# Performance work log

Measured on AMD Instinct MI355X. Metric: run time of the kernel, lower is better.

## Reference

```python
import jax, jax.numpy as jnp
import numpy as np

# ---------- static mesh topology helpers (numpy, setup-time only) ----------

def _topo_subdivide(nv, faces):
    edge_id = {}
    mids = []
    nf = []
    def mid(a, b):
        k = (a, b) if a < b else (b, a)
        if k not in edge_id:
            edge_id[k] = nv + len(mids)
            mids.append(k)
        return edge_id[k]
    for a, b, c in faces:
        a, b, c = int(a), int(b), int(c)
        ab, bc, ca = mid(a, b), mid(b, c), mid(c, a)
        nf += [[a, ab, ca], [b, bc, ab], [c, ca, bc], [ab, bc, ca]]
    return np.array(nf, dtype=np.int64), np.array(mids, dtype=np.int64)

def _icosphere(level, radius):
    t = (1.0 + 5.0 ** 0.5) / 2.0
    v = np.array([[-1, t, 0], [1, t, 0], [-1, -t, 0], [1, -t, 0],
                  [0, -1, t], [0, 1, t], [0, -1, -t], [0, 1, -t],
                  [t, 0, -1], [t, 0, 1], [-t, 0, -1], [-t, 0, 1]], dtype=np.float64)
    v /= np.linalg.norm(v, axis=1, keepdims=True)
    f = np.array([[0, 11, 5], [0, 5, 1], [0, 1, 7], [0, 7, 10], [0, 10, 11],
                  [1, 5, 9], [5, 11, 4], [11, 10, 2], [10, 7, 6], [7, 1, 8],
                  [3, 9, 4], [3, 4, 2], [3, 2, 6], [3, 6, 8], [3, 8, 9],
                  [4, 9, 5], [2, 4, 11], [6, 2, 10], [8, 6, 7], [9, 8, 1]], dtype=np.int64)
    for _ in range(level):
        f, mids = _topo_subdivide(len(v), f)
        mv = v[mids[:, 0]] + v[mids[:, 1]]
        mv /= np.linalg.norm(mv, axis=1, keepdims=True)
        v = np.concatenate([v, mv], 0)
    return (v * radius).astype(np.float32), f

def _directed_edges(faces):
    e = np.concatenate([faces[:, [0, 1]], faces[:, [1, 2]], faces[:, [2, 0]],
                        faces[:, [1, 0]], faces[:, [2, 1]], faces[:, [0, 2]]], 0)
    return np.unique(e, axis=0).T.astype(np.int64)  # (2, E) directed, deduped

# ---------- jax forward math ----------

def _project(verts, camera_c, camera_f):
    # K @ [I | t], t = (0,0,0.8): rows [f0,0,c0,0.8*c0],[0,f1,c1,0.8*c1],[0,0,1,0.8]
    z = jnp.zeros((), verts.dtype); o = jnp.ones((), verts.dtype)
    tz = jnp.asarray(0.8, verts.dtype)
    P = jnp.stack([
        jnp.stack([camera_f[0], z, camera_c[0], tz * camera_c[0]]),
        jnp.stack([z, camera_f[1], camera_c[1], tz * camera_c[1]]),
        jnp.stack([z, z, o, tz])])
    hom = jnp.concatenate([verts, jnp.ones((verts.shape[0], 1), verts.dtype)], 1)
    pc = hom @ P.T                     # (V, 3)
    return pc[:, :2] / pc[:, 2:3]      # (V, 2) pixel coords [x, y]

def _bilerp(feat, px, py, image_size):
    # feat: (C, dim, dim); px, py: (V,)
    dim = feat.shape[1]
    x = px * dim / image_size
    y = py * dim / image_size
    x1 = jnp.floor(x); x2 = x1 + 1.0
    y1 = jnp.floor(y); y2 = y1 + 1.0
    xi1 = jnp.clip(x1.astype(jnp.int32), 0, dim - 1)
    xi2 = jnp.clip(x2.astype(jnp.int32), 0, dim - 1)
    yi1 = jnp.clip(y1.astype(jnp.int32), 0, dim - 1)
    yi2 = jnp.clip(y2.astype(jnp.int32), 0, dim - 1)
    f11 = feat[:, xi1, yi1].T  # (V, C)
    f12 = feat[:, xi1, yi2].T
    f21 = feat[:, xi2, yi1].T
    f22 = feat[:, xi2, yi2].T
    w11 = ((x2 - x) * (y2 - y))[:, None]
    w12 = ((x2 - x) * (y - y1))[:, None]
    w21 = ((x - x1) * (y2 - y))[:, None]
    w22 = ((x - x1) * (y - y1))[:, None]
    return w11 * f11 + w12 * f12 + w21 * f21 + w22 * f22

def _gconv(x, W0, W1, b, src, dst):
    agg = jax.ops.segment_sum(x[dst], src, num_segments=x.shape[0])
    return x @ W0 + agg @ W1 + b

def _gresnet(x, edges, params):
    Win0, Win1, bin_, W0s, W1s, bs, Wc0, Wc1, bc = params
    src, dst = edges[0], edges[1]
    h = jax.nn.relu(_gconv(x, Win0, Win1, bin_, src, dst))
    def body(h, lw):
        W0, W1, b = lw
        return jax.nn.relu(_gconv(h, W0, W1, b, src, dst)) + h, None
    h, _ = jax.lax.scan(body, h, (W0s, W1s, bs))
    coords = _gconv(h, Wc0, Wc1, bc, src, dst)
    return h, coords

def _forward(f3, f4, f5, verts0, camera_c, camera_f, p1, p2, p3,
             edges1, edges2, edges3, mid0, mid1, image_size):
    def deform(verts, shape_feat, edges, params):
        pix = _project(verts, camera_c, camera_f)
        px, py = pix[:, 0], pix[:, 1]
        perc = jnp.concatenate([_bilerp(f3, px, py, image_size),
                                _bilerp(f4, px, py, image_size),
                                _bilerp(f5, px, py, image_size)], 1)  # (V, 1280)
        feats = jnp.concatenate([perc, shape_feat], 1)
        h, coords = _gresnet(feats, edges, params)
        return coords, h
    def unpool(verts, feat, mid):
        vf = jnp.concatenate([verts, feat], 1)
        new = (vf[mid[:, 0]] + vf[mid[:, 1]]) * 0.5  # edge midpoints
        vf = jnp.concatenate([vf, new], 0)
        return vf[:, :3], vf[:, 3:]
    verts, feat = deform(verts0, verts0, edges1, p1)
    verts, feat = unpool(verts, feat, mid0)
    verts, feat = deform(verts, feat, edges2, p2)
    verts, feat = unpool(verts, feat, mid1)
    verts, _ = deform(verts, feat, edges3, p3)
    return verts  # (40962, 3)

# ---------- harness entry points ----------

def setup_inputs() -> dict:
    key = jax.random.key(0)
    keys = iter(jax.random.split(key, 64))
    v0, f0 = _icosphere(4, 0.2)                      # 2562 verts, 5120 faces
    f1, mid0 = _topo_subdivide(len(v0), f0)          # -> 10242 verts topology
    f2, mid1 = _topo_subdivide(len(v0) + len(mid0), f1)  # -> 40962 verts
    inp = {
        'f3': jax.random.normal(next(keys), (256, 56, 56), jnp.float32),
        'f4': jax.random.normal(next(keys), (512, 28, 28), jnp.float32),
        'f5': jax.random.normal(next(keys), (512, 14, 14), jnp.float32),
        'verts0': jnp.asarray(v0),
        'camera_c': jnp.array([112.0, 112.0], jnp.float32),
        'camera_f': jnp.array([248.0, 248.0], jnp.float32),
    }
    D, L = 128, 12
    def stage(prefix, in_dim):
        def w(shape, scale):
            return jax.random.normal(next(keys), shape, jnp.float32) * scale
        inp[prefix + '_Win0'] = w((in_dim, D), 1.0 / np.sqrt(in_dim))
        inp[prefix + '_Win1'] = w((in_dim, D), 1.0 / np.sqrt(in_dim))
        inp[prefix + '_bin'] = jnp.zeros((D,), jnp.float32)
        inp[prefix + '_W0'] = w((L, D, D), 0.3 / np.sqrt(D))
        inp[prefix + '_W1'] = w((L, D, D), 0.3 / np.sqrt(D))
        inp[prefix + '_b'] = jnp.zeros((L, D), jnp.float32)
        inp[prefix + '_Wc0'] = w((D, 3), 0.01 / np.sqrt(D))
        inp[prefix + '_Wc1'] = w((D, 3), 0.01 / np.sqrt(D))
        inp[prefix + '_bc'] = jnp.zeros((3,), jnp.float32)
    stage('g1', 1283)
    stage('g2', 1408)
    stage('g3', 1408)
    inp['edges1'] = jnp.asarray(_directed_edges(f0))   # (2, 15360)
    inp['edges2'] = jnp.asarray(_directed_edges(f1))   # (2, 61440)
    inp['edges3'] = jnp.asarray(_directed_edges(f2))   # (2, 245760)
    inp['mid0'] = jnp.asarray(mid0)                    # (7680, 2)
    inp['mid1'] = jnp.asarray(mid1)                    # (30720, 2)
    inp['image_size'] = 224
    return inp

def reference(f3, f4, f5, verts0, camera_c, camera_f,
              g1_Win0, g1_Win1, g1_bin, g1_W0, g1_W1, g1_b, g1_Wc0, g1_Wc1, g1_bc,
              g2_Win0, g2_Win1, g2_bin, g2_W0, g2_W1, g2_b, g2_Wc0, g2_Wc1, g2_bc,
              g3_Win0, g3_Win1, g3_bin, g3_W0, g3_W1, g3_b, g3_Wc0, g3_Wc1, g3_bc,
              edges1, edges2, edges3, mid0, mid1, image_size):
    p1 = (g1_Win0, g1_Win1, g1_bin, g1_W0, g1_W1, g1_b, g1_Wc0, g1_Wc1, g1_bc)
    p2 = (g2_Win0, g2_Win1, g2_bin, g2_W0, g2_W1, g2_b, g2_Wc0, g2_Wc1, g2_bc)
    p3 = (g3_Win0, g3_Win1, g3_bin, g3_W0, g3_W1, g3_b, g3_Wc0, g3_Wc1, g3_bc)
    return _forward(f3, f4, f5, verts0, camera_c, camera_f, p1, p2, p3,
                    edges1, edges2, edges3, mid0, mid1, image_size)
```

## Files before the change

kernel.cpp:

```cpp
#include <hip/hip_runtime.h>
#include <hip/hip_bf16.h>
#include <cstddef>
#include <cstdint>

#define DIV_UP(a, b) (((a) + (b) - 1) / (b))

typedef __attribute__((ext_vector_type(8))) short bf16x8v;
typedef __attribute__((ext_vector_type(4))) float f32x4v;

__device__ __forceinline__ unsigned short bf16_rn(float v) {
    unsigned int u = __float_as_uint(v);
    unsigned int r = (u + 0x7FFFu + ((u >> 16) & 1u)) >> 16;
    return (unsigned short)r;
}
__device__ __forceinline__ float bf16_f(unsigned short h) {
    return __uint_as_float(((unsigned int)h) << 16);
}
__device__ __forceinline__ void f2hl(float v, unsigned short& hi, unsigned short& lo) {
    hi = bf16_rn(v);
    float r = v - bf16_f(hi);
    lo = bf16_rn(r);
}
__device__ __forceinline__ int xcd_swz(int orig, int nwg) {
    int q = nwg >> 3, r = nwg & 7;
    int xcd = orig & 7, idx = orig >> 3;
    return (xcd < r ? xcd * (q + 1) : r * (q + 1) + (xcd - r) * q) + idx;
}

__global__ void transpose_hl(const float* __restrict__ in, unsigned short* __restrict__ ohi,
                             unsigned short* __restrict__ olo, int C, int HW) {
    int idx = blockIdx.x * 256 + threadIdx.x;
    if (idx >= C * HW) return;
    int c = idx % C;
    int p = idx / C;
    float v = in[(size_t)c * HW + p];
    unsigned short hi, lo;
    f2hl(v, hi, lo);
    ohi[(size_t)p * C + c] = hi;
    olo[(size_t)p * C + c] = lo;
}

struct PackArgs {
    const float* Win0[3]; const float* Win1[3];
    const float* W0L[3];  const float* W1L[3];
    unsigned short* BtLp[3];
    unsigned short *BtShi[2], *BtSlo[2];
    unsigned short *Bgh[3], *Bgl[3];
};

__global__ void pack_all(PackArgs p) {
    const int LAY1 = 12 * 32768;
    const int LAYT = 3 * LAY1;
    const int SH1 = 256 * 128;
    const int SHT = 2 * SH1;
    const int GB0 = 768 * 256, GB1 = 768 * 512;
    int idx = blockIdx.x * 256 + threadIdx.x;
    if (idx < LAYT) {
        int st = idx / LAY1, r = idx % LAY1;
        int layer = r >> 15, q = r & 32767;
        int ks = q >> 12, nt = (q >> 9) & 7, lane = (q >> 3) & 63, i = q & 7;
        int n = nt * 16 + (lane & 15);
        int k = ks * 32 + ((lane >> 4) << 3) + i;
        float v = (k < 128) ? p.W0L[st][(size_t)layer * 16384 + k * 128 + n]
                            : p.W1L[st][(size_t)layer * 16384 + (k - 128) * 128 + n];
        unsigned short hi, lo;
        f2hl(v, hi, lo);
        size_t base = ((size_t)layer * 64 + ks * 8 + nt) * 1024 + lane * 8 + i;
        p.BtLp[st][base] = hi;
        p.BtLp[st][base + 512] = lo;
        return;
    }
    float v;
    unsigned short* dh;
    unsigned short* dl;
    size_t o;
    if (idx < LAYT + SHT) {
        int q = idx - LAYT;
        int st = q / SH1, rr = q % SH1;
        int n = rr >> 7, k = rr & 127;
        const float* w0 = p.Win0[st + 1];
        const float* w1 = p.Win1[st + 1];
        v = (n < 128) ? w0[(size_t)(1280 + k) * 128 + n]
                      : w1[(size_t)(1280 + k) * 128 + (n - 128)];
        dh = p.BtShi[st]; dl = p.BtSlo[st]; o = rr;
    } else {
        int q = idx - LAYT - SHT;
        int m, C, base;
        if (q < GB0) { m = 0; C = 256; base = 0; }
        else if (q < GB0 + GB1) { m = 1; C = 512; base = 256; q -= GB0; }
        else if (q < GB0 + 2 * GB1) { m = 2; C = 512; base = 768; q -= GB0 + GB1; }
        else return;
        int n = q / C, k = q % C;
        int s = n >> 8, j = n & 255;
        v = (j < 128) ? p.Win0[s][(size_t)(base + k) * 128 + j]
                      : p.Win1[s][(size_t)(base + k) * 128 + (j - 128)];
        dh = p.Bgh[m]; dl = p.Bgl[m]; o = q;
    }
    unsigned short hi, lo;
    f2hl(v, hi, lo);
    dh[o] = hi;
    dl[o] = lo;
}

__global__ void desc_adj_kernel(const float* __restrict__ verts,
                                const float* __restrict__ cam_c, const float* __restrict__ cam_f,
                                const int* __restrict__ imgsz, int V,
                                const int* __restrict__ src, const int* __restrict__ dst, int E,
                                int* __restrict__ sampi, float* __restrict__ sampw,
                                int* __restrict__ adj8) {
    int v = blockIdx.x * 256 + threadIdx.x;
    if (v >= V) return;
    float X = verts[3 * v + 0], Yy = verts[3 * v + 1], Z = verts[3 * v + 2];
    float cx = cam_c[0], cy = cam_c[1], fx = cam_f[0], fy = cam_f[1];
    const float tz = 0.8f;
    float pz = Z + tz;
    float px = (fx * X + cx * Z + tz * cx) / pz;
    float py = (fy * Yy + cy * Z + tz * cy) / pz;
    float is = (float)imgsz[0];
    const int Ss[3] = {56, 28, 14};
#pragma unroll
    for (int m = 0; m < 3; ++m) {
        int S = Ss[m];
        float dim = (float)S;
        float x = px * dim / is;
        float y = py * dim / is;
        float x1 = floorf(x), y1 = floorf(y);
        float x2 = x1 + 1.0f, y2 = y1 + 1.0f;
        float smax = (float)(S - 1);
        int xi1 = (int)fminf(fmaxf(x1, 0.0f), smax);
        int xi2 = (int)fminf(fmaxf(x2, 0.0f), smax);
        int yi1 = (int)fminf(fmaxf(y1, 0.0f), smax);
        int yi2 = (int)fminf(fmaxf(y2, 0.0f), smax);
        int b = v * 12 + m * 4;
        sampi[b + 0] = xi1 * S + yi1;
        sampi[b + 1] = xi1 * S + yi2;
        sampi[b + 2] = xi2 * S + yi1;
        sampi[b + 3] = xi2 * S + yi2;
        sampw[b + 0] = (x2 - x) * (y2 - y);
        sampw[b + 1] = (x2 - x) * (y - y1);
        sampw[b + 2] = (x - x1) * (y2 - y);
        sampw[b + 3] = (x - x1) * (y - y1);
    }
    int lo = 0, hi = E;
    while (lo < hi) { int m = (lo + hi) >> 1; if (src[m] < v) lo = m + 1; else hi = m; }
    int e0 = lo;
    hi = E;
    while (lo < hi) { int m = (lo + hi) >> 1; if (src[m] < v + 1) lo = m + 1; else hi = m; }
    int e1 = lo;
    int* ap = adj8 + (size_t)v * 8;
#pragma unroll
    for (int i = 0; i < 8; ++i) {
        int e = e0 + i;
        ap[i] = (e < e1) ? dst[e] : -1;
    }
}

struct MArgs {
    const unsigned short *Ahi, *Alo; int lda;
    const unsigned short *Bhi, *Blo; int K;
    float* Y;
    int sstr;
    int V;
};

template <int EPI>
__global__ __launch_bounds__(256) void mgemm(MArgs g) {
    __shared__ unsigned short As_hi[64][40], As_lo[64][40];
    __shared__ unsigned short Bs_hi[128][40], Bs_lo[128][40];
    int tid = threadIdx.x;
    int row0 = blockIdx.y * 64;
    int col0 = blockIdx.x * 128;
    int l = tid & 63, wid = tid >> 6;
    int wr = wid & 1, wc = wid >> 1;
    int lw = l & 15, gg = l >> 4;
    f32x4v acc[2][4];
#pragma unroll
    for (int i = 0; i < 2; ++i)
#pragma unroll
        for (int j = 0; j < 4; ++j) acc[i][j] = (f32x4v){0.f, 0.f, 0.f, 0.f};

    int arow = tid >> 2, akoff = (tid & 3) * 8;
    for (int k0 = 0; k0 < g.K; k0 += 32) {
        __syncthreads();
        {
            int grow = row0 + arow;
            uint4 zh = make_uint4(0, 0, 0, 0), zl = make_uint4(0, 0, 0, 0);
            if (grow < g.V) {
                zh = *(const uint4*)(g.Ahi + (size_t)grow * g.lda + k0 + akoff);
                zl = *(const uint4*)(g.Alo + (size_t)grow * g.lda + k0 + akoff);
            }
            *(uint4*)&As_hi[arow][akoff] = zh;
            *(uint4*)&As_lo[arow][akoff] = zl;
        }
#pragma unroll
        for (int it = 0; it < 2; ++it) {
            int q = tid + it * 256;
            int n = q >> 2, koff = (q & 3) * 8;
            *(uint4*)&Bs_hi[n][koff] = *(const uint4*)(g.Bhi + (size_t)(col0 + n) * g.K + k0 + koff);
            *(uint4*)&Bs_lo[n][koff] = *(const uint4*)(g.Blo + (size_t)(col0 + n) * g.K + k0 + koff);
        }
        __syncthreads();
        bf16x8v ah[2], al[2], bh[4], bl[4];
#pragma unroll
        for (int mt = 0; mt < 2; ++mt) {
            int r = wr * 32 + mt * 16 + lw;
            ah[mt] = *(const bf16x8v*)&As_hi[r][gg * 8];
            al[mt] = *(const bf16x8v*)&As_lo[r][gg * 8];
        }
#pragma unroll
        for (int nt = 0; nt < 4; ++nt) {
            int c = wc * 64 + nt * 16 + lw;
            bh[nt] = *(const bf16x8v*)&Bs_hi[c][gg * 8];
            bl[nt] = *(const bf16x8v*)&Bs_lo[c][gg * 8];
        }
#pragma unroll
        for (int mt = 0; mt < 2; ++mt)
#pragma unroll
            for (int nt = 0; nt < 4; ++nt) {
                acc[mt][nt] = __builtin_amdgcn_mfma_f32_16x16x32_bf16(ah[mt], bh[nt], acc[mt][nt], 0, 0, 0);
                acc[mt][nt] = __builtin_amdgcn_mfma_f32_16x16x32_bf16(ah[mt], bl[nt], acc[mt][nt], 0, 0, 0);
                acc[mt][nt] = __builtin_amdgcn_mfma_f32_16x16x32_bf16(al[mt], bh[nt], acc[mt][nt], 0, 0, 0);
            }
    }
#pragma unroll
    for (int mt = 0; mt < 2; ++mt)
#pragma unroll
        for (int nt = 0; nt < 4; ++nt) {
            int colg = wc * 64 + nt * 16 + lw;
#pragma unroll
            for (int r = 0; r < 4; ++r) {
                int rowg = row0 + wr * 32 + mt * 16 + gg * 4 + r;
                if (rowg >= g.V) continue;
                float v = acc[mt][nt][r];
                if (EPI == 3) {
                    g.Y[(size_t)rowg * 256 + col0 + colg] = v;
                } else {
                    int cg = col0 + colg;
                    g.Y[(size_t)(cg >> 8) * g.sstr + (size_t)rowg * 256 + (cg & 255)] = v;
                }
            }
        }
}

__global__ void gather_kernel(const float* __restrict__ G, int sstr,
                              const int* __restrict__ sampi, const float* __restrict__ sampw,
                              float* __restrict__ Yb, int V, int stage,
                              const float* __restrict__ Win0, const float* __restrict__ Win1,
                              const float* __restrict__ shape) {
    int v = xcd_swz(blockIdx.x, gridDim.x) * 4 + (threadIdx.x >> 6);
    if (v >= V) return;
    int j = (threadIdx.x & 63) * 4;
    const float* Gs = G + (size_t)stage * sstr;
    int b = v * 12;
    float4 acc;
    if (stage == 0) acc = make_float4(0.f, 0.f, 0.f, 0.f);
    else acc = *(const float4*)(Yb + (size_t)v * 256 + j);
#pragma unroll
    for (int s = 0; s < 4; ++s) {
        float w = sampw[b + s];
        float4 f = *(const float4*)(Gs + (size_t)sampi[b + s] * 256 + j);
        acc.x += w * f.x; acc.y += w * f.y; acc.z += w * f.z; acc.w += w * f.w;
    }
#pragma unroll
    for (int s = 0; s < 4; ++s) {
        float w = sampw[b + 4 + s];
        float4 f = *(const float4*)(Gs + (size_t)(3136 + sampi[b + 4 + s]) * 256 + j);
        acc.x += w * f.x; acc.y += w * f.y; acc.z += w * f.z; acc.w += w * f.w;
    }
#pragma unroll
    for (int s = 0; s < 4; ++s) {
        float w = sampw[b + 8 + s];
        float4 f = *(const float4*)(Gs + (size_t)(3920 + sampi[b + 8 + s]) * 256 + j);
        acc.x += w * f.x; acc.y += w * f.y; acc.z += w * f.z; acc.w += w * f.w;
    }
    if (stage == 0) {
#pragma unroll
        for (int k = 0; k < 3; ++k) {
            float w = shape[v * 3 + k];
            const float* wr = (j < 128) ? Win0 + (size_t)(1280 + k) * 128 + j
                                        : Win1 + (size_t)(1280 + k) * 128 + (j - 128);
            float4 wv = *(const float4*)wr;
            acc.x += w * wv.x; acc.y += w * wv.y; acc.z += w * wv.z; acc.w += w * wv.w;
        }
    }
    *(float4*)(Yb + (size_t)v * 256 + j) = acc;
}

__global__ __launch_bounds__(256) void combine_in(
    const float* __restrict__ Y, const float* __restrict__ bias,
    const int* __restrict__ adj8,
    float* __restrict__ hout, int V) {
    int v = xcd_swz(blockIdx.x, gridDim.x) * 8 + (threadIdx.x >> 5);
    if (v >= V) return;
    int d = (threadIdx.x & 31) * 4;
    float4 val = *(const float4*)(Y + (size_t)v * 256 + d);
    float4 b4 = *(const float4*)(bias + d);
    val.x += b4.x; val.y += b4.y; val.z += b4.z; val.w += b4.w;
    const int* ap = adj8 + (size_t)v * 8;
    int n[6];
#pragma unroll
    for (int i = 0; i < 6; ++i) n[i] = ap[i];
#pragma unroll
    for (int i = 0; i < 6; ++i) {
        if (n[i] >= 0) {
            float4 f = *(const float4*)(Y + (size_t)n[i] * 256 + 128 + d);
            val.x += f.x; val.y += f.y; val.z += f.z; val.w += f.w;
        }
    }
    val.x = fmaxf(val.x, 0.f); val.y = fmaxf(val.y, 0.f);
    val.z = fmaxf(val.z, 0.f); val.w = fmaxf(val.w, 0.f);
    *(float4*)(hout + (size_t)v * 128 + d) = val;
}

struct LArgs {
    const float* h;
    const unsigned short* Bp;
    const int* adj8;
    const float* bias;
    float* hnext;
    int V;
};

__global__ __launch_bounds__(256, 4) void lay_kernel(LArgs g) {
    __shared__ float psA[16][132];
    __shared__ float psB[16][132];
    int tid = threadIdx.x;
    int wid = tid >> 6, l = tid & 63;
    int role_k = wid & 1, role_n = wid >> 1;
    int rowbase = xcd_swz(blockIdx.x, gridDim.x) * 16;
    int lrow = l & 15, lks = l >> 4;
    int grow = rowbase + lrow;
    bool act = grow < g.V;

    f32x4v acc[4];
#pragma unroll
    for (int nt = 0; nt < 4; ++nt) acc[nt] = (f32x4v){0.f, 0.f, 0.f, 0.f};

    if (role_k == 0) {
        const float* hp = g.h + (size_t)grow * 128;
#pragma unroll
        for (int ks = 0; ks < 4; ++ks) {
            int kb = ks * 32 + lks * 8;
            float a[8];
            if (act) {
                float4 f0 = *(const float4*)(hp + kb);
                float4 f1 = *(const float4*)(hp + kb + 4);
                a[0] = f0.x; a[1] = f0.y; a[2] = f0.z; a[3] = f0.w;
                a[4] = f1.x; a[5] = f1.y; a[6] = f1.z; a[7] = f1.w;
            } else {
#pragma unroll
                for (int i = 0; i < 8; ++i) a[i] = 0.f;
            }
            unsigned short hh[8], ll[8];
#pragma unroll
            for (int i = 0; i < 8; ++i) f2hl(a[i], hh[i], ll[i]);
            bf16x8v ah = *(const bf16x8v*)hh;
            bf16x8v al = *(const bf16x8v*)ll;
#pragma unroll
            for (int nt = 0; nt < 4; ++nt) {
                int ntg = role_n * 4 + nt;
                const unsigned short* p = g.Bp + (size_t)(ks * 8 + ntg) * 1024 + l * 8;
                bf16x8v bh = *(const bf16x8v*)p;
                bf16x8v bl = *(const bf16x8v*)(p + 512);
                acc[nt] = __builtin_amdgcn_mfma_f32_16x16x32_bf16(ah, bh, acc[nt], 0, 0, 0);
                acc[nt] = __builtin_amdgcn_mfma_f32_16x16x32_bf16(ah, bl, acc[nt], 0, 0, 0);
                acc[nt] = __builtin_amdgcn_mfma_f32_16x16x32_bf16(al, bh, acc[nt], 0, 0, 0);
            }
        }
    } else {
        int n[6];
        if (act) {
            const int* ap = g.adj8 + (size_t)grow * 8;
#pragma unroll
            for (int i = 0; i < 6; ++i) n[i] = ap[i];
        } else {
#pragma unroll
            for (int i = 0; i < 6; ++i) n[i] = -1;
        }
#pragma unroll
        for (int ks = 0; ks < 4; ++ks) {
            int ko = ks * 32 + lks * 8;
            float a[8];
#pragma unroll
            for (int i = 0; i < 8; ++i) a[i] = 0.f;
#pragma unroll
            for (int i = 0; i < 6; ++i) {
                if (n[i] >= 0) {
                    const float* hp = g.h + (size_t)n[i] * 128 + ko;
                    float4 f0 = *(const float4*)hp;
                    float4 f1 = *(const float4*)(hp + 4);
                    a[0] += f0.x; a[1] += f0.y; a[2] += f0.z; a[3] += f0.w;
                    a[4] += f1.x; a[5] += f1.y; a[6] += f1.z; a[7] += f1.w;
                }
            }
            unsigned short hh[8], ll[8];
#pragma unroll
            for (int i = 0; i < 8; ++i) f2hl(a[i], hh[i], ll[i]);
            bf16x8v ah = *(const bf16x8v*)hh;
            bf16x8v al = *(const bf16x8v*)ll;
#pragma unroll
            for (int nt = 0; nt < 4; ++nt) {
                int ntg = role_n * 4 + nt;
                const unsigned short* p = g.Bp + (size_t)((ks + 4) * 8 + ntg) * 1024 + l * 8;
                bf16x8v bh = *(const bf16x8v*)p;
                bf16x8v bl = *(const bf16x8v*)(p + 512);
                acc[nt] = __builtin_amdgcn_mfma_f32_16x16x32_bf16(ah, bh, acc[nt], 0, 0, 0);
                acc[nt] = __builtin_amdgcn_mfma_f32_16x16x32_bf16(ah, bl, acc[nt], 0, 0, 0);
                acc[nt] = __builtin_amdgcn_mfma_f32_16x16x32_bf16(al, bh, acc[nt], 0, 0, 0);
            }
        }
    }

    {
        float(*ps)[132] = role_k ? psA : psB;
#pragma unroll
        for (int nt = 0; nt < 4; ++nt) {
            int col = role_n * 64 + nt * 16 + lrow;
#pragma unroll
            for (int r = 0; r < 4; ++r) ps[lks * 4 + r][col] = acc[nt][r];
        }
    }
    __syncthreads();

    int erow = tid >> 5;
    int ecol = (tid & 31) * 4;
    float4 b4 = *(const float4*)(g.bias + ecol);
#pragma unroll
    for (int rr = 0; rr < 2; ++rr) {
        int row = rr * 8 + erow;
        int rowg = rowbase + row;
        if (rowg < g.V) {
            float4 s;
            s.x = psA[row][ecol + 0] + psB[row][ecol + 0] + b4.x;
            s.y = psA[row][ecol + 1] + psB[row][ecol + 1] + b4.y;
            s.z = psA[row][ecol + 2] + psB[row][ecol + 2] + b4.z;
            s.w = psA[row][ecol + 3] + psB[row][ecol + 3] + b4.w;
            s.x = fmaxf(s.x, 0.f); s.y = fmaxf(s.y, 0.f);
            s.z = fmaxf(s.z, 0.f); s.w = fmaxf(s.w, 0.f);
            float4 hres = *(const float4*)(g.h + (size_t)rowg * 128 + ecol);
            s.x += hres.x; s.y += hres.y; s.z += hres.z; s.w += hres.w;
            *(float4*)(g.hnext + (size_t)rowg * 128 + ecol) = s;
        }
    }
}

__global__ void coordgemm_kernel(const float* __restrict__ h,
                                 const float* __restrict__ Wc0, const float* __restrict__ Wc1,
                                 int V, float* __restrict__ Yc) {
    int idx = blockIdx.x * 256 + threadIdx.x;
    if (idx >= V * 6) return;
    int v = idx / 6, j = idx % 6;
    const float* W = (j < 3) ? Wc0 : Wc1;
    int jj = (j < 3) ? j : j - 3;
    const float* hp = h + (size_t)v * 128;
    float acc = 0.0f;
#pragma unroll
    for (int k = 0; k < 32; ++k) {
        float4 f = *(const float4*)(hp + k * 4);
        acc += f.x * W[(k * 4 + 0) * 3 + jj];
        acc += f.y * W[(k * 4 + 1) * 3 + jj];
        acc += f.z * W[(k * 4 + 2) * 3 + jj];
        acc += f.w * W[(k * 4 + 3) * 3 + jj];
    }
    Yc[idx] = acc;
}

__global__ void coordcombine_kernel(const float* __restrict__ Yc, const float* __restrict__ bc,
                                    const int* __restrict__ adj8,
                                    int V, float* __restrict__ out) {
    int idx = blockIdx.x * 256 + threadIdx.x;
    if (idx >= V * 3) return;
    int v = idx / 3, j = idx % 3;
    float val = Yc[(size_t)v * 6 + j] + bc[j];
    const int* ap = adj8 + (size_t)v * 8;
    int n[6];
#pragma unroll
    for (int i = 0; i < 6; ++i) n[i] = ap[i];
#pragma unroll
    for (int i = 0; i < 6; ++i)
        if (n[i] >= 0) val += Yc[(size_t)n[i] * 6 + 3 + j];
    out[(size_t)v * 3 + j] = val;
}

__global__ void unpool_kernel(float* __restrict__ verts, const float* __restrict__ h,
                              const int* __restrict__ mid, int V, int Nm,
                              unsigned short* __restrict__ fphi, unsigned short* __restrict__ fplo) {
    int r = blockIdx.x;
    int t = threadIdx.x;
    if (r < V) {
        float v = h[(size_t)r * 128 + t];
        unsigned short hi, lo;
        f2hl(v, hi, lo);
        fphi[(size_t)r * 128 + t] = hi;
        fplo[(size_t)r * 128 + t] = lo;
    } else {
        int i = r - V;
        int a = mid[2 * i], b = mid[2 * i + 1];
        float v = 0.5f * (h[(size_t)a * 128 + t] + h[(size_t)b * 128 + t]);
        unsigned short hi, lo;
        f2hl(v, hi, lo);
        fphi[(size_t)r * 128 + t] = hi;
        fplo[(size_t)r * 128 + t] = lo;
        if (t < 3)
            verts[(size_t)r * 3 + t] = 0.5f * (verts[(size_t)a * 3 + t] + verts[(size_t)b * 3 + t]);
    }
}

extern "C" void kernel_launch(void* const* d_in, const int* in_sizes, int n_in,
                              void* d_out, int out_size, void* d_ws, size_t ws_size,
                              hipStream_t stream) {
    const float* f3 = (const float*)d_in[0];
    const float* f4 = (const float*)d_in[1];
    const float* f5 = (const float*)d_in[2];
    const float* verts0 = (const float*)d_in[3];
    const float* cam_c = (const float*)d_in[4];
    const float* cam_f = (const float*)d_in[5];
    const int* imgsz = (const int*)d_in[38];

    int V0 = in_sizes[3] / 3;
    int E[3] = {in_sizes[33] / 2, in_sizes[34] / 2, in_sizes[35] / 2};
    int Nm0 = in_sizes[36] / 2, Nm1 = in_sizes[37] / 2;
    int V1 = V0 + Nm0, V2 = V1 + Nm1;
    int Vs[3] = {V0, V1, V2};
    const int NPIXT = 3136 + 784 + 196;
    const int GS = NPIXT * 256;

    char* wsp = (char*)d_ws;
    auto alloc = [&](size_t bytes) -> void* {
        void* p = (void*)wsp;
        wsp += (bytes + 255) & ~(size_t)255;
        return p;
    };
    unsigned short* ft0h = (unsigned short*)alloc((size_t)3136 * 256 * 2);
    unsigned short* ft0l = (unsigned short*)alloc((size_t)3136 * 256 * 2);
    unsigned short* ft1h = (unsigned short*)alloc((size_t)784 * 512 * 2);
    unsigned short* ft1l = (unsigned short*)alloc((size_t)784 * 512 * 2);
    unsigned short* ft2h = (unsigned short*)alloc((size_t)196 * 512 * 2);
    unsigned short* ft2l = (unsigned short*)alloc((size_t)196 * 512 * 2);
    unsigned short* Bg0h = (unsigned short*)alloc((size_t)768 * 256 * 2);
    unsigned short* Bg0l = (unsigned short*)alloc((size_t)768 * 256 * 2);
    unsigned short* Bg1h = (unsigned short*)alloc((size_t)768 * 512 * 2);
    unsigned short* Bg1l = (unsigned short*)alloc((size_t)768 * 512 * 2);
    unsigned short* Bg2h = (unsigned short*)alloc((size_t)768 * 512 * 2);
    unsigned short* Bg2l = (unsigned short*)alloc((size_t)768 * 512 * 2);
    float* Gbuf = (float*)alloc((size_t)3 * GS * 4);
    unsigned short* BtLp[3];
    for (int s = 0; s < 3; ++s)
        BtLp[s] = (unsigned short*)alloc((size_t)12 * 65536 * 2);
    unsigned short* BtShi[2];
    unsigned short* BtSlo[2];
    for (int s = 0; s < 2; ++s) {
        BtShi[s] = (unsigned short*)alloc((size_t)256 * 128 * 2);
        BtSlo[s] = (unsigned short*)alloc((size_t)256 * 128 * 2);
    }
    float* Ybuf = (float*)alloc((size_t)V2 * 256 * 4);
    float* hA = (float*)alloc((size_t)V2 * 128 * 4);
    float* hB = (float*)alloc((size_t)V2 * 128 * 4);
    unsigned short* FPhi = (unsigned short*)alloc((size_t)V2 * 128 * 2);
    unsigned short* FPlo = (unsigned short*)alloc((size_t)V2 * 128 * 2);
    float* vertsbuf = (float*)alloc((size_t)V2 * 3 * 4);
    float* Yc = (float*)alloc((size_t)V2 * 6 * 4);
    int* sampi = (int*)alloc((size_t)V2 * 12 * 4);
    float* sampw = (float*)alloc((size_t)V2 * 12 * 4);
    int* adj8 = (int*)alloc((size_t)V2 * 8 * 4);

    transpose_hl<<<DIV_UP(256 * 56 * 56, 256), 256, 0, stream>>>(f3, ft0h, ft0l, 256, 56 * 56);
    transpose_hl<<<DIV_UP(512 * 28 * 28, 256), 256, 0, stream>>>(f4, ft1h, ft1l, 512, 28 * 28);
    transpose_hl<<<DIV_UP(512 * 14 * 14, 256), 256, 0, stream>>>(f5, ft2h, ft2l, 512, 14 * 14);

    {
        PackArgs p;
        for (int s = 0; s < 3; ++s) {
            p.Win0[s] = (const float*)d_in[6 + s * 9 + 0];
            p.Win1[s] = (const float*)d_in[6 + s * 9 + 1];
            p.W0L[s] = (const float*)d_in[6 + s * 9 + 3];
            p.W1L[s] = (const float*)d_in[6 + s * 9 + 4];
            p.BtLp[s] = BtLp[s];
        }
        p.BtShi[0] = BtShi[0]; p.BtSlo[0] = BtSlo[0];
        p.BtShi[1] = BtShi[1]; p.BtSlo[1] = BtSlo[1];
        p.Bgh[0] = Bg0h; p.Bgl[0] = Bg0l;
        p.Bgh[1] = Bg1h; p.Bgl[1] = Bg1l;
        p.Bgh[2] = Bg2h; p.Bgl[2] = Bg2l;
        int total = 3 * 12 * 32768 + 2 * 256 * 128 + 768 * 256 + 2 * 768 * 512;
        pack_all<<<DIV_UP(total, 256), 256, 0, stream>>>(p);
    }

    {
        MArgs m = {};
        m.sstr = GS;
        m.Ahi = ft0h; m.Alo = ft0l; m.lda = 256;
        m.Bhi = Bg0h; m.Blo = Bg0l; m.K = 256;
        m.Y = Gbuf; m.V = 3136;
        dim3 g0(6, DIV_UP(3136, 64));
        mgemm<2><<<g0, 256, 0, stream>>>(m);
        m.Ahi = ft1h; m.Alo = ft1l; m.lda = 512;
        m.Bhi = Bg1h; m.Blo = Bg1l; m.K = 512;
        m.Y = Gbuf + (size_t)3136 * 256; m.V = 784;
        dim3 g1(6, DIV_UP(784, 64));
        mgemm<2><<<g1, 256, 0, stream>>>(m);
        m.Ahi = ft2h; m.Alo = ft2l; m.lda = 512;
        m.Bhi = Bg2h; m.Blo = Bg2l; m.K = 512;
        m.Y = Gbuf + (size_t)3920 * 256; m.V = 196;
        dim3 g2(6, DIV_UP(196, 64));
        mgemm<2><<<g2, 256, 0, stream>>>(m);
    }

    for (int si = 0; si < 3; ++si) {
        const float* Win0 = (const float*)d_in[6 + si * 9 + 0];
        const float* Win1 = (const float*)d_in[6 + si * 9 + 1];
        const float* bin = (const float*)d_in[6 + si * 9 + 2];
        const float* bs = (const float*)d_in[6 + si * 9 + 5];
        const float* Wc0 = (const float*)d_in[6 + si * 9 + 6];
        const float* Wc1 = (const float*)d_in[6 + si * 9 + 7];
        const float* bc = (const float*)d_in[6 + si * 9 + 8];
        const int* edges = (const int*)d_in[33 + si];
        int Ecur = E[si];
        const int* esrc = edges;
        const int* edst = edges + Ecur;
        int V = Vs[si];
        const float* vertsin = (si == 0) ? verts0 : vertsbuf;

        desc_adj_kernel<<<DIV_UP(V, 256), 256, 0, stream>>>(vertsin, cam_c, cam_f, imgsz, V,
                                                            esrc, edst, Ecur, sampi, sampw, adj8);
        if (si > 0) {
            MArgs m = {};
            m.Ahi = FPhi; m.Alo = FPlo; m.lda = 128;
            m.Bhi = BtShi[si - 1]; m.Blo = BtSlo[si - 1]; m.K = 128;
            m.Y = Ybuf; m.V = V;
            dim3 grid(2, DIV_UP(V, 64));
            mgemm<3><<<grid, 256, 0, stream>>>(m);
        }
        gather_kernel<<<DIV_UP(V, 4), 256, 0, stream>>>(Gbuf, GS, sampi, sampw, Ybuf, V, si,
                                                        Win0, Win1, (si == 0) ? verts0 : nullptr);
        combine_in<<<DIV_UP(V, 8), 256, 0, stream>>>(Ybuf, bin, adj8, hA, V);

        float* hcur = hA;
        float* hnext = hB;
        for (int ll = 0; ll < 12; ++ll) {
            LArgs a = {};
            a.h = hcur;
            a.Bp = BtLp[si] + (size_t)ll * 65536;
            a.adj8 = adj8;
            a.bias = bs + (size_t)ll * 128;
            a.hnext = hnext;
            a.V = V;
            lay_kernel<<<DIV_UP(V, 16), 256, 0, stream>>>(a);
            float* t = hcur; hcur = hnext; hnext = t;
        }

        coordgemm_kernel<<<DIV_UP(V * 6, 256), 256, 0, stream>>>(hcur, Wc0, Wc1, V, Yc);
        float* ctarget = (si == 2) ? (float*)d_out : vertsbuf;
        coordcombine_kernel<<<DIV_UP(V * 3, 256), 256, 0, stream>>>(Yc, bc, adj8, V, ctarget);
        if (si < 2) {
            const int* mid = (const int*)d_in[36 + si];
            int Nm = (si == 0) ? Nm0 : Nm1;
            unpool_kernel<<<V + Nm, 128, 0, stream>>>(vertsbuf, hcur, mid, V, Nm, FPhi, FPlo);
        }
    }
}
```

Before: 1.385 ms.

## Prefetch neighbor rows branchlessly via zero pad row in graph layer kernel

```diff
diff --git a/kernel.cpp b/kernel.cpp
--- a/kernel.cpp
+++ b/kernel.cpp
@@ -155,6 +155,12 @@
     }
 }
 
+__global__ void zero_pad(float* __restrict__ a, float* __restrict__ b) {
+    int t = threadIdx.x;
+    a[t] = 0.0f;
+    b[t] = 0.0f;
+}
+
 struct MArgs {
     const unsigned short *Ahi, *Alo; int lda;
     const unsigned short *Bhi, *Blo; int K;
@@ -321,7 +327,7 @@
     int V;
 };
 
-__global__ __launch_bounds__(256, 4) void lay_kernel(LArgs g) {
+__global__ __launch_bounds__(256, 2) void lay_kernel(LArgs g) {
     __shared__ float psA[16][132];
     __shared__ float psB[16][132];
     int tid = threadIdx.x;
@@ -336,79 +342,79 @@
 #pragma unroll
     for (int nt = 0; nt < 4; ++nt) acc[nt] = (f32x4v){0.f, 0.f, 0.f, 0.f};
 
+    auto domfma = [&](const float* a, int ksg) {
+        unsigned short hh[8], ll[8];
+#pragma unroll
+        for (int i = 0; i < 8; ++i) f2hl(a[i], hh[i], ll[i]);
+        bf16x8v ah = *(const bf16x8v*)hh;
+        bf16x8v al = *(const bf16x8v*)ll;
+#pragma unroll
+        for (int nt = 0; nt < 4; ++nt) {
+            int ntg = role_n * 4 + nt;
+            const unsigned short* p = g.Bp + (size_t)(ksg * 8 + ntg) * 1024 + l * 8;
+            bf16x8v bh = *(const bf16x8v*)p;
+            bf16x8v bl = *(const bf16x8v*)(p + 512);
+            acc[nt] = __builtin_amdgcn_mfma_f32_16x16x32_bf16(ah, bh, acc[nt], 0, 0, 0);
+            acc[nt] = __builtin_amdgcn_mfma_f32_16x16x32_bf16(ah, bl, acc[nt], 0, 0, 0);
+            acc[nt] = __builtin_amdgcn_mfma_f32_16x16x32_bf16(al, bh, acc[nt], 0, 0, 0);
+        }
+    };
+
     if (role_k == 0) {
-        const float* hp = g.h + (size_t)grow * 128;
+        const float* hp = g.h + (size_t)(act ? grow : g.V) * 128 + lks * 8;
+        float4 own[8];
 #pragma unroll
         for (int ks = 0; ks < 4; ++ks) {
-            int kb = ks * 32 + lks * 8;
+            own[ks * 2] = *(const float4*)(hp + ks * 32);
+            own[ks * 2 + 1] = *(const float4*)(hp + ks * 32 + 4);
+        }
+#pragma unroll
+        for (int ks = 0; ks < 4; ++ks) {
             float a[8];
-            if (act) {
-                float4 f0 = *(const float4*)(hp + kb);
-                float4 f1 = *(const float4*)(hp + kb + 4);
-                a[0] = f0.x; a[1] = f0.y; a[2] = f0.z; a[3] = f0.w;
-                a[4] = f1.x; a[5] = f1.y; a[6] = f1.z; a[7] = f1.w;
-            } else {
-#pragma unroll
-                for (int i = 0; i < 8; ++i) a[i] = 0.f;
+            *(float4*)&a[0] = own[ks * 2];
+            *(float4*)&a[4] = own[ks * 2 + 1];
+            domfma(a, ks);
+        }
+    } else {
+        const float* hp[6];
+        {
+            const int* ap = g.adj8 + (size_t)grow * 8;
+#pragma unroll
+            for (int i = 0; i < 6; ++i) {
+                int t = act ? ap[i] : -1;
+                int nb = (t >= 0) ? t : g.V;
+                hp[i] = g.h + (size_t)nb * 128 + lks * 8;
             }
-            unsigned short hh[8], ll[8];
-#pragma unroll
-            for (int i = 0; i < 8; ++i) f2hl(a[i], hh[i], ll[i]);
-            bf16x8v ah = *(const bf16x8v*)hh;
-            bf16x8v al = *(const bf16x8v*)ll;
-#pragma unroll
-            for (int nt = 0; nt < 4; ++nt) {
-                int ntg = role_n * 4 + nt;
-                const unsigned short* p = g.Bp + (size_t)(ks * 8 + ntg) * 1024 + l * 8;
-                bf16x8v bh = *(const bf16x8v*)p;
-                bf16x8v bl = *(const bf16x8v*)(p + 512);
-                acc[nt] = __builtin_amdgcn_mfma_f32_16x16x32_bf16(ah, bh, acc[nt], 0, 0, 0);
-                acc[nt] = __builtin_amdgcn_mfma_f32_16x16x32_bf16(ah, bl, acc[nt], 0, 0, 0);
-                acc[nt] = __builtin_amdgcn_mfma_f32_16x16x32_bf16(al, bh, acc[nt], 0, 0, 0);
+        }
+        float4 bufA[12], bufB[12];
+        auto issue = [&](float4* buf, int ks) {
+#pragma unroll
+            for (int i = 0; i < 6; ++i) {
+                buf[i * 2] = *(const float4*)(hp[i] + ks * 32);
+                buf[i * 2 + 1] = *(const float4*)(hp[i] + ks * 32 + 4);
             }
-        }
-    } else {
-        int n[6];
-        if (act) {
-            const int* ap = g.adj8 + (size_t)grow * 8;
-#pragma unroll
-            for (int i = 0; i < 6; ++i) n[i] = ap[i];
-        } else {
-#pragma unroll
-            for (int i = 0; i < 6; ++i) n[i] = -1;
-        }
-#pragma unroll
-        for (int ks = 0; ks < 4; ++ks) {
-            int ko = ks * 32 + lks * 8;
+        };
+        auto consume = [&](const float4* buf, int ks) {
             float a[8];
 #pragma unroll
             for (int i = 0; i < 8; ++i) a[i] = 0.f;
 #pragma unroll
             for (int i = 0; i < 6; ++i) {
-                if (n[i] >= 0) {
-                    const float* hp = g.h + (size_t)n[i] * 128 + ko;
-                    float4 f0 = *(const float4*)hp;
-                    float4 f1 = *(const float4*)(hp + 4);
-                    a[0] += f0.x; a[1] += f0.y; a[2] += f0.z; a[3] += f0.w;
-                    a[4] += f1.x; a[5] += f1.y; a[6] += f1.z; a[7] += f1.w;
-                }
+                a[0] += buf[i * 2].x; a[1] += buf[i * 2].y;
+                a[2] += buf[i * 2].z; a[3] += buf[i * 2].w;
+                a[4] += buf[i * 2 + 1].x; a[5] += buf[i * 2 + 1].y;
+                a[6] += buf[i * 2 + 1].z; a[7] += buf[i * 2 + 1].w;
             }
-            unsigned short hh[8], ll[8];
-#pragma unroll
-            for (int i = 0; i < 8; ++i) f2hl(a[i], hh[i], ll[i]);
-            bf16x8v ah = *(const bf16x8v*)hh;
-            bf16x8v al = *(const bf16x8v*)ll;
-#pragma unroll
-            for (int nt = 0; nt < 4; ++nt) {
-                int ntg = role_n * 4 + nt;
-                const unsigned short* p = g.Bp + (size_t)((ks + 4) * 8 + ntg) * 1024 + l * 8;
-                bf16x8v bh = *(const bf16x8v*)p;
-                bf16x8v bl = *(const bf16x8v*)(p + 512);
-                acc[nt] = __builtin_amdgcn_mfma_f32_16x16x32_bf16(ah, bh, acc[nt], 0, 0, 0);
-                acc[nt] = __builtin_amdgcn_mfma_f32_16x16x32_bf16(ah, bl, acc[nt], 0, 0, 0);
-                acc[nt] = __builtin_amdgcn_mfma_f32_16x16x32_bf16(al, bh, acc[nt], 0, 0, 0);
-            }
-        }
+            domfma(a, 4 + ks);
+        };
+        issue(bufA, 0);
+        issue(bufB, 1);
+        consume(bufA, 0);
+        issue(bufA, 2);
+        consume(bufB, 1);
+        issue(bufB, 3);
+        consume(bufA, 2);
+        consume(bufB, 3);
     }
 
     {
@@ -554,8 +560,8 @@
         BtSlo[s] = (unsigned short*)alloc((size_t)256 * 128 * 2);
     }
     float* Ybuf = (float*)alloc((size_t)V2 * 256 * 4);
-    float* hA = (float*)alloc((size_t)V2 * 128 * 4);
-    float* hB = (float*)alloc((size_t)V2 * 128 * 4);
+    float* hA = (float*)alloc(((size_t)V2 + 8) * 128 * 4);
+    float* hB = (float*)alloc(((size_t)V2 + 8) * 128 * 4);
     unsigned short* FPhi = (unsigned short*)alloc((size_t)V2 * 128 * 2);
     unsigned short* FPlo = (unsigned short*)alloc((size_t)V2 * 128 * 2);
     float* vertsbuf = (float*)alloc((size_t)V2 * 3 * 4);
@@ -623,6 +629,7 @@
 
         desc_adj_kernel<<<DIV_UP(V, 256), 256, 0, stream>>>(vertsin, cam_c, cam_f, imgsz, V,
                                                             esrc, edst, Ecur, sampi, sampw, adj8);
+        zero_pad<<<1, 128, 0, stream>>>(hA + (size_t)V * 128, hB + (size_t)V * 128);
         if (si > 0) {
             MArgs m = {};
             m.Ahi = FPhi; m.Alo = FPlo; m.lda = 128;
```

Result: faster. 1.328 ms (-4.1%).
